# Performance work log

Measured on AMD Instinct MI355X. Metric: run time of the kernel, lower is better.

The kernel has to match this reference:

```python
import jax, jax.numpy as jnp
import numpy as np

# AdaMixer AdaptiveMixing config
G = 4          # n_groups
P_IN = 32      # in_points
P_OUT = 128    # out_points
C_EFF = 64     # eff_in_dim == eff_out_dim (in_dim=out_dim=256 / G)
DQ = 256       # query_dim
M_PARAMS = C_EFF * C_EFF      # 4096
S_PARAMS = P_IN * P_OUT       # 4096
TOTAL = M_PARAMS + S_PARAMS   # 8192
EPS = 1e-5


def setup_inputs() -> dict:
    key = jax.random.key(0)
    k = jax.random.split(key, 6)
    B, N = 8, 500
    x = jax.random.normal(k[0], (B, N, G, P_IN, C_EFF), dtype=jnp.float32)
    query = jax.random.normal(k[1], (B, N, DQ), dtype=jnp.float32)
    # parameter generator Linear(DQ -> G*TOTAL). (Original inits weight to zero;
    # we use small random weights so the computation is non-degenerate.)
    Wp = jax.random.normal(k[2], (G * TOTAL, DQ), dtype=jnp.float32) * 0.02
    bp = jax.random.normal(k[3], (G * TOTAL,), dtype=jnp.float32) * 0.02
    # out_proj Linear(G*P_OUT*C_EFF -> DQ)
    Wo = jax.random.normal(k[4], (DQ, G * P_OUT * C_EFF), dtype=jnp.float32) * 0.02
    bo = jax.random.normal(k[5], (DQ,), dtype=jnp.float32) * 0.02
    return {"x": x, "query": query, "Wp": Wp, "bp": bp, "Wo": Wo, "bo": bo}


def _ln2(t):
    # LayerNorm over last two axes, no affine (F.layer_norm(out, [P, C]))
    mean = jnp.mean(t, axis=(-2, -1), keepdims=True)
    var = jnp.var(t, axis=(-2, -1), keepdims=True)
    return (t - mean) * jax.lax.rsqrt(var + EPS)


def reference(x, query, Wp, bp, Wo, bo):
    B, N = query.shape[:2]
    # generate per-query mixing parameters: [B, N, G*TOTAL]
    params = jnp.einsum('bnd,pd->bnp', query, Wp) + bp
    params = params.reshape(B, N, G, TOTAL)
    M = params[..., :M_PARAMS].reshape(B, N, G, C_EFF, C_EFF)
    S = params[..., M_PARAMS:].reshape(B, N, G, P_OUT, P_IN)
    # adaptive channel mixing: [B,N,G,P_in,C] @ [B,N,G,C,C]
    out = jnp.einsum('bngpc,bngcd->bngpd', x, M)
    out = jax.nn.relu(_ln2(out))
    # adaptive spatial mixing: [B,N,G,P_out,P_in] @ [B,N,G,P_in,C]
    out = jnp.einsum('bngop,bngpc->bngoc', S, out)
    out = jax.nn.relu(_ln2(out))
    # output projection back to query dim + residual
    out = out.reshape(B, N, G * P_OUT * C_EFF)
    out = jnp.einsum('bnf,df->bnd', out, Wo) + bo
    return query + out
```

## Files before the change

kernel.cpp:

```cpp
#include <hip/hip_runtime.h>

typedef __attribute__((ext_vector_type(8))) __bf16 bf16x8;
typedef __attribute__((ext_vector_type(4))) float f32x4;
typedef __attribute__((ext_vector_type(8))) unsigned short u16x8;
typedef __attribute__((ext_vector_type(4))) unsigned short u16x4;
typedef unsigned int u32;

#define KS2 32

__device__ __forceinline__ unsigned short f2b(float f) {
    union { float f; unsigned u; } v; v.f = f;
    unsigned r = v.u + 0x7fffu + ((v.u >> 16) & 1u);
    return (unsigned short)(r >> 16);
}

__device__ __forceinline__ float b2f(unsigned short b) {
    union { unsigned u; float f; } v; v.u = ((unsigned)b) << 16;
    return v.f;
}

__device__ __forceinline__ bf16x8 ld_frag(const unsigned short* p) {
    u16x8 v = *(const u16x8*)p;
    return __builtin_bit_cast(bf16x8, v);
}

__device__ __forceinline__ void gl16(void* lds, const void* g) {
    __builtin_amdgcn_global_load_lds(
        (const __attribute__((address_space(1))) u32*)g,
        (__attribute__((address_space(3))) u32*)lds, 16, 0, 0);
}

#define WAIT_VM0 asm volatile("s_waitcnt vmcnt(0)" ::: "memory")
#define WAIT_VM3 asm volatile("s_waitcnt vmcnt(3)" ::: "memory")
#define WAIT_VM6 asm volatile("s_waitcnt vmcnt(6)" ::: "memory")
#define WAIT_LG0 asm volatile("s_waitcnt lgkmcnt(0)" ::: "memory")
#define BARRIER  __builtin_amdgcn_s_barrier()

__device__ __forceinline__ int inv_col(int j) {
    int off = j & 8191;
    return (off < 4096) ? ((j & ~8191) | ((off & 63) << 6) | (off >> 6)) : j;
}

__device__ __forceinline__ void block_reduce2(float& s, float& q, float* red) {
    for (int m = 1; m < 64; m <<= 1) { s += __shfl_xor(s, m); q += __shfl_xor(q, m); }
    int w = threadIdx.x >> 6;
    __syncthreads();
    if ((threadIdx.x & 63) == 0) { red[w] = s; red[w + 4] = q; }
    __syncthreads();
    s = red[0] + red[1] + red[2] + red[3];
    q = red[4] + red[5] + red[6] + red[7];
}

__global__ __launch_bounds__(256) void k_cvt(const float* __restrict__ src,
                                             unsigned short* __restrict__ dst, int n4) {
    int i = blockIdx.x * 256 + threadIdx.x;
    int stride = gridDim.x * 256;
    for (; i < n4; i += stride) {
        f32x4 v = *(const f32x4*)&src[(size_t)i * 4];
        u16x4 o = { f2b(v[0]), f2b(v[1]), f2b(v[2]), f2b(v[3]) };
        *(u16x4*)&dst[(size_t)i * 4] = o;
    }
}

__global__ __launch_bounds__(256) void k_cvt_wp(const float* __restrict__ Wp,
                                                unsigned short* __restrict__ Wpb, int n4) {
    int i = blockIdx.x * 256 + threadIdx.x;
    int stride = gridDim.x * 256;
    for (; i < n4; i += stride) {
        int e = i * 4;
        int j = e >> 8, k = e & 255;
        int jo = inv_col(j);
        f32x4 v = *(const f32x4*)&Wp[(size_t)jo * 256 + k];
        u16x4 o = { f2b(v[0]), f2b(v[1]), f2b(v[2]), f2b(v[3]) };
        *(u16x4*)&Wpb[(size_t)e] = o;
    }
}

__global__ __launch_bounds__(256) void k_perm_bp(const float* __restrict__ bp,
                                                 float* __restrict__ bpp) {
    int j = blockIdx.x * 256 + threadIdx.x;
    bpp[j] = bp[inv_col(j)];
}


__global__ __launch_bounds__(512) void k_gemm1(
    const unsigned short* __restrict__ qb, const unsigned short* __restrict__ Wpb,
    const float* __restrict__ bpp, unsigned short* __restrict__ pm, int CH)
{
    __shared__ char SB[73728];
    const int t = threadIdx.x, lane = t & 63, w = t >> 6;
    const int l15 = lane & 15, k8 = lane >> 4;
    const int n0 = blockIdx.x * 128, m0 = blockIdx.y * 256;
    const int wm = (w >> 1) * 64, wn = (w & 1) * 64;

    f32x4 acc[4][4];
    for (int i = 0; i < 4; ++i)
        for (int j = 0; j < 4; ++j) acc[i][j] = (f32x4){0.f, 0.f, 0.f, 0.f};

    const int r0 = t >> 2;
    const int cbs = (((t & 3) ^ (r0 & 3)) * 16);
    int ma0 = m0 + r0;        if (ma0 > CH - 1) ma0 = CH - 1;
    int ma1 = m0 + r0 + 128;  if (ma1 > CH - 1) ma1 = CH - 1;
    const char* pa0 = (const char*)qb  + (size_t)ma0 * 512 + cbs;
    const char* pa1 = (const char*)qb  + (size_t)ma1 * 512 + cbs;
    const char* pb0 = (const char*)Wpb + (size_t)(n0 + r0) * 512 + cbs;

    char* cur = SB;
    char* nx1 = SB + 24576;
    char* nx2 = SB + 49152;

    gl16(cur + t * 16,         pa0);
    gl16(cur + 8192 + t * 16,  pa1);
    gl16(cur + 16384 + t * 16, pb0);
    gl16(nx1 + t * 16,         pa0 + 64);
    gl16(nx1 + 8192 + t * 16,  pa1 + 64);
    gl16(nx1 + 16384 + t * 16, pb0 + 64);

    for (int kt = 0; kt < 8; ++kt) {
        if (kt < 6) {
            const int kb = (kt + 2) * 64;
            gl16(nx2 + t * 16,         pa0 + kb);
            gl16(nx2 + 8192 + t * 16,  pa1 + kb);
            gl16(nx2 + 16384 + t * 16, pb0 + kb);
            WAIT_VM6;
        } else if (kt == 6) {
            WAIT_VM3;
        } else {
            WAIT_VM0;
        }
        BARRIER;
        const unsigned short* Ab = (const unsigned short*)cur;
        const unsigned short* Bb = (const unsigned short*)(cur + 16384);
        bf16x8 a[4], b[4];
        for (int mi = 0; mi < 4; ++mi) {
            int row = wm + mi * 16 + l15;
            a[mi] = ld_frag(&Ab[row * 32 + (k8 ^ (row & 3)) * 8]);
        }
        for (int ni = 0; ni < 4; ++ni) {
            int row = wn + ni * 16 + l15;
            b[ni] = ld_frag(&Bb[row * 32 + (k8 ^ (row & 3)) * 8]);
        }
        WAIT_LG0;
        for (int mi = 0; mi < 4; ++mi)
            for (int ni = 0; ni < 4; ++ni)
                acc[mi][ni] = __builtin_amdgcn_mfma_f32_16x16x32_bf16(a[mi], b[ni], acc[mi][ni], 0, 0, 0);
        BARRIER;
        char* tmp = cur; cur = nx1; nx1 = nx2; nx2 = tmp;
    }

    unsigned short* Ep = (unsigned short*)SB;
    for (int ni = 0; ni < 4; ++ni) {
        int col = wn + ni * 16 + l15;
        float bpv = bpp[n0 + col];
        for (int mi = 0; mi < 4; ++mi)
            for (int r = 0; r < 4; ++r) {
                int row = wm + mi * 16 + k8 * 4 + r;
                Ep[row * 128 + col] = f2b(acc[mi][ni][r] + bpv);
            }
    }
    __syncthreads();
    for (int i = 0; i < 8; ++i) {
        int off = t * 16 + i * 8192;
        int row = off >> 8, colb = off & 255;
        int cm = m0 + row;
        if (cm < CH)
            *(u16x8*)((char*)pm + (size_t)cm * 65536 + (size_t)n0 * 2 + colb) =
                *(const u16x8*)((const char*)SB + off);
    }
}

__global__ __launch_bounds__(256) void k_mix(
    const float* __restrict__ x, unsigned short* __restrict__ pm, int q0)
{
    __shared__ char SB[29184];
    __shared__ float red[8];
    unsigned short* MtP = (unsigned short*)SB;
    unsigned short* Ax  = (unsigned short*)(SB + 9216);
    unsigned short* Ss  = (unsigned short*)(SB + 13824);
    unsigned short* O1  = (unsigned short*)(SB + 24064);
    unsigned short* O2  = (unsigned short*)SB;
    const int t = threadIdx.x, lane = t & 63, w = t >> 6;
    const int l15 = lane & 15, k8 = lane >> 4;
    const int g = blockIdx.x, nq = blockIdx.y;
    unsigned short* pmq = pm + (size_t)nq * 32768 + g * 8192;
    const float* xg = x + ((size_t)(q0 + nq) * 4 + g) * 2048;

    {
        int d = t >> 2, c0 = (t & 3) * 16;
        u16x8 v0 = *(const u16x8*)&pmq[d * 64 + c0];
        u16x8 v1 = *(const u16x8*)&pmq[d * 64 + c0 + 8];
        *(u16x8*)&MtP[d * 72 + c0] = v0;
        *(u16x8*)&MtP[d * 72 + c0 + 8] = v1;
    }
    {
        int o = t >> 1, p0 = (t & 1) * 16;
        u16x8 v0 = *(const u16x8*)&pmq[4096 + o * 32 + p0];
        u16x8 v1 = *(const u16x8*)&pmq[4096 + o * 32 + p0 + 8];
        *(u16x8*)&Ss[o * 40 + p0] = v0;
        *(u16x8*)&Ss[o * 40 + p0 + 8] = v1;
    }
    {
        int p = t >> 3, c0 = (t & 7) * 8;
        f32x4 v0 = *(const f32x4*)&xg[p * 64 + c0];
        f32x4 v1 = *(const f32x4*)&xg[p * 64 + c0 + 4];
        u16x8 o8 = { f2b(v0[0]), f2b(v0[1]), f2b(v0[2]), f2b(v0[3]),
                     f2b(v1[0]), f2b(v1[1]), f2b(v1[2]), f2b(v1[3]) };
        *(u16x8*)&Ax[p * 72 + c0] = o8;
    }
    __syncthreads();

    f32x4 acc1[2] = { (f32x4){0.f,0.f,0.f,0.f}, (f32x4){0.f,0.f,0.f,0.f} };
    for (int kk = 0; kk < 2; ++kk) {
        bf16x8 b = ld_frag(&MtP[(16 * w + l15) * 72 + kk * 32 + k8 * 8]);
        for (int mi = 0; mi < 2; ++mi) {
            bf16x8 a = ld_frag(&Ax[(mi * 16 + l15) * 72 + kk * 32 + k8 * 8]);
            acc1[mi] = __builtin_amdgcn_mfma_f32_16x16x32_bf16(a, b, acc1[mi], 0, 0, 0);
        }
    }
    float s = 0.f, sq = 0.f;
    for (int mi = 0; mi < 2; ++mi)
        for (int r = 0; r < 4; ++r) { float v = acc1[mi][r]; s += v; sq += v * v; }
    block_reduce2(s, sq, red);
    float mean = s * (1.f / 2048.f);
    float inv = rsqrtf(sq * (1.f / 2048.f) - mean * mean + 1e-5f);
    for (int mi = 0; mi < 2; ++mi)
        for (int r = 0; r < 4; ++r) {
            float v = (acc1[mi][r] - mean) * inv; v = fmaxf(v, 0.f);
            int p = mi * 16 + k8 * 4 + r, d = 16 * w + l15;
            O1[d * 40 + p] = f2b(v);
        }
    __syncthreads();

    f32x4 acc2[8];
    for (int mi = 0; mi < 8; ++mi) acc2[mi] = (f32x4){0.f, 0.f, 0.f, 0.f};
    bf16x8 b2 = ld_frag(&O1[(16 * w + l15) * 40 + k8 * 8]);
    for (int mi = 0; mi < 8; ++mi) {
        bf16x8 a2 = ld_frag(&Ss[(mi * 16 + l15) * 40 + k8 * 8]);
        acc2[mi] = __builtin_amdgcn_mfma_f32_16x16x32_bf16(a2, b2, acc2[mi], 0, 0, 0);
    }
    s = 0.f; sq = 0.f;
    for (int mi = 0; mi < 8; ++mi)
        for (int r = 0; r < 4; ++r) { float v = acc2[mi][r]; s += v; sq += v * v; }
    block_reduce2(s, sq, red);
    mean = s * (1.f / 8192.f);
    inv = rsqrtf(sq * (1.f / 8192.f) - mean * mean + 1e-5f);
    for (int mi = 0; mi < 8; ++mi)
        for (int r = 0; r < 4; ++r) {
            float v = (acc2[mi][r] - mean) * inv; v = fmaxf(v, 0.f);
            int o = mi * 16 + k8 * 4 + r, d = 16 * w + l15;
            O2[o * 64 + d] = f2b(v);
        }
    __syncthreads();
    for (int i = 0; i < 4; ++i) {
        int off = t * 16 + i * 4096;
        *(u16x8*)((char*)pmq + off) = *(const u16x8*)((const char*)O2 + off);
    }
}

__global__ __launch_bounds__(512) void k_gemm2(
    const unsigned short* __restrict__ pm, const unsigned short* __restrict__ Wob,
    unsigned short* __restrict__ part, int CH)
{
    __shared__ char SB[73728];
    const int t = threadIdx.x, lane = t & 63, w = t >> 6;
    const int l15 = lane & 15, k8 = lane >> 4;
    const int m0 = blockIdx.x * 128;
    const int ks = blockIdx.y;
    const int ksb = ks * (65536 / KS2);
    const int wm = (w >> 2) * 64, wn = (w & 3) * 64;

    f32x4 acc[4][4];
    for (int i = 0; i < 4; ++i)
        for (int j = 0; j < 4; ++j) acc[i][j] = (f32x4){0.f, 0.f, 0.f, 0.f};

    const int r0 = t >> 2;
    const int cbs = (((t & 3) ^ (r0 & 3)) * 16);
    int ma = m0 + r0; if (ma > CH - 1) ma = CH - 1;
    const char* pa  = (const char*)pm  + (size_t)ma * 65536 + ksb + cbs;
    const char* pb0 = (const char*)Wob + (size_t)r0 * 65536 + ksb + cbs;
    const char* pb1 = pb0 + (size_t)128 * 65536;

    char* cur = SB;
    char* nx1 = SB + 24576;
    char* nx2 = SB + 49152;

    gl16(cur + t * 16,          pa);
    gl16(cur + 8192 + t * 16,   pb0);
    gl16(cur + 16384 + t * 16,  pb1);
    gl16(nx1 + t * 16,          pa + 64);
    gl16(nx1 + 8192 + t * 16,   pb0 + 64);
    gl16(nx1 + 16384 + t * 16,  pb1 + 64);

    const int NT = (65536 / KS2) / 64;
    for (int kt = 0; kt < NT; ++kt) {
        if (kt < NT - 2) {
            const int kb = (kt + 2) * 64;
            gl16(nx2 + t * 16,         pa  + kb);
            gl16(nx2 + 8192 + t * 16,  pb0 + kb);
            gl16(nx2 + 16384 + t * 16, pb1 + kb);
            WAIT_VM6;
        } else if (kt == NT - 2) {
            WAIT_VM3;
        } else {
            WAIT_VM0;
        }
        BARRIER;
        const unsigned short* Ab = (const unsigned short*)cur;
        const unsigned short* Bb = (const unsigned short*)(cur + 8192);
        bf16x8 a[4], b[4];
        for (int mi = 0; mi < 4; ++mi) {
            int row = wm + mi * 16 + l15;
            a[mi] = ld_frag(&Ab[row * 32 + (k8 ^ (row & 3)) * 8]);
        }
        for (int ni = 0; ni < 4; ++ni) {
            int row = wn + ni * 16 + l15;
            b[ni] = ld_frag(&Bb[row * 32 + (k8 ^ (row & 3)) * 8]);
        }
        WAIT_LG0;
        for (int mi = 0; mi < 4; ++mi)
            for (int ni = 0; ni < 4; ++ni)
                acc[mi][ni] = __builtin_amdgcn_mfma_f32_16x16x32_bf16(a[mi], b[ni], acc[mi][ni], 0, 0, 0);
        BARRIER;
        char* tmp = cur; cur = nx1; nx1 = nx2; nx2 = tmp;
    }

    for (int mi = 0; mi < 4; ++mi)
        for (int ni = 0; ni < 4; ++ni)
            for (int r = 0; r < 4; ++r) {
                int row = wm + mi * 16 + k8 * 4 + r;
                int cm = m0 + row;
                int d = wn + ni * 16 + l15;
                if (cm < CH) part[((size_t)ks * CH + cm) * 256 + d] = f2b(acc[mi][ni][r]);
            }
}

__global__ __launch_bounds__(256) void k_reduce(
    const unsigned short* __restrict__ part, const float* __restrict__ query,
    const float* __restrict__ bo, float* __restrict__ out, int q0, int CH)
{
    int row = blockIdx.x * 4 + (threadIdx.x >> 6);
    if (row >= CH) return;
    int d4 = (threadIdx.x & 63) * 4;
    f32x4 s = *(const f32x4*)&bo[d4];
    f32x4 qv = *(const f32x4*)&query[(size_t)(q0 + row) * 256 + d4];
    s = s + qv;
    for (int ks = 0; ks < KS2; ++ks) {
        u16x4 p4 = *(const u16x4*)&part[((size_t)ks * CH + row) * 256 + d4];
        s[0] += b2f(p4[0]); s[1] += b2f(p4[1]); s[2] += b2f(p4[2]); s[3] += b2f(p4[3]);
    }
    *(f32x4*)&out[(size_t)(q0 + row) * 256 + d4] = s;
}

extern "C" void kernel_launch(void* const* d_in, const int* in_sizes, int n_in,
                              void* d_out, int out_size, void* d_ws, size_t ws_size,
                              hipStream_t stream) {
    const float* x     = (const float*)d_in[0];
    const float* query = (const float*)d_in[1];
    const float* Wp    = (const float*)d_in[2];
    const float* bp    = (const float*)d_in[3];
    const float* Wo    = (const float*)d_in[4];
    const float* bo    = (const float*)d_in[5];
    float* out = (float*)d_out;

    char* ws = (char*)d_ws;
    unsigned short* Wpb = (unsigned short*)ws;
    unsigned short* Wob = (unsigned short*)(ws + 16777216);
    unsigned short* qb  = (unsigned short*)(ws + 33554432);
    float*          bpp = (float*)(ws + 35602432);
    char* chunkbase = ws + 35733504;
    const size_t fixed = 35733504;

    static const int cands[] = {2000, 1000, 500, 250, 200, 125, 100, 50, 25, 20, 10, 8, 5, 4, 2, 1};
    int CH = 1;
    for (int i = 0; i < (int)(sizeof(cands) / sizeof(cands[0])); ++i) {
        size_t need = fixed + (size_t)cands[i] * (65536 + (size_t)KS2 * 512);
        if (need <= ws_size) { CH = cands[i]; break; }
    }
    unsigned short* pm = (unsigned short*)chunkbase;
    unsigned short* part = (unsigned short*)(chunkbase + (size_t)CH * 65536);
    const int NC = 4000 / CH;

    k_perm_bp<<<128, 256, 0, stream>>>(bp, bpp);
    k_cvt_wp<<<2048, 256, 0, stream>>>(Wp, Wpb, 32768 * 256 / 4);
    k_cvt<<<2048, 256, 0, stream>>>(Wo, Wob, 256 * 32768 / 4);
    k_cvt<<<1000, 256, 0, stream>>>(query, qb, 4000 * 256 / 4);

    for (int c = 0; c < NC; ++c) {
        int q0 = c * CH;
        k_gemm1<<<dim3(256, (CH + 255) / 256), 512, 0, stream>>>(
            qb + (size_t)q0 * 256, Wpb, bpp, pm, CH);
        k_mix<<<dim3(4, CH), 256, 0, stream>>>(x, pm, q0);
        k_gemm2<<<dim3((CH + 127) / 128, KS2), 512, 0, stream>>>(pm, Wob, part, CH);
        k_reduce<<<dim3((CH + 3) / 4), 256, 0, stream>>>(part, query, bo, out, q0, CH);
    }
}
```

Measured before the change: 349.8 us.

## Enlarge gemm2 M tile to 256 and map K-splits to XCDs

The output-projection split-K GEMM now uses a 256-row M tile per block (8x4 MFMA accumulators per wave) instead of 128, so each Wo tile loaded into LDS serves twice as many rows. The grid is flattened to 1D and remapped so that consecutive block IDs, which land on different XCDs, take different K-splits while blocks sharing a K-split share an XCD and its L2. This cuts Wo global traffic and block count, at the cost of more accumulator registers, more LDS (96KB), and fewer blocks, which can lower occupancy.

After: 353.2 us. About the same (+1.0%).

```diff
diff --git a/kernel.cpp b/kernel.cpp
--- a/kernel.cpp
+++ b/kernel.cpp
@@ -32,7 +32,9 @@
 
 #define WAIT_VM0 asm volatile("s_waitcnt vmcnt(0)" ::: "memory")
 #define WAIT_VM3 asm volatile("s_waitcnt vmcnt(3)" ::: "memory")
+#define WAIT_VM4 asm volatile("s_waitcnt vmcnt(4)" ::: "memory")
 #define WAIT_VM6 asm volatile("s_waitcnt vmcnt(6)" ::: "memory")
+#define WAIT_VM8 asm volatile("s_waitcnt vmcnt(8)" ::: "memory")
 #define WAIT_LG0 asm volatile("s_waitcnt lgkmcnt(0)" ::: "memory")
 #define BARRIER  __builtin_amdgcn_s_barrier()
 
@@ -259,56 +261,63 @@
 
 __global__ __launch_bounds__(512) void k_gemm2(
     const unsigned short* __restrict__ pm, const unsigned short* __restrict__ Wob,
-    unsigned short* __restrict__ part, int CH)
+    unsigned short* __restrict__ part, int CH, int MB2)
 {
-    __shared__ char SB[73728];
+    __shared__ char SB[98304];
     const int t = threadIdx.x, lane = t & 63, w = t >> 6;
     const int l15 = lane & 15, k8 = lane >> 4;
-    const int m0 = blockIdx.x * 128;
-    const int ks = blockIdx.y;
+    const int bid = blockIdx.x;
+    const int xcd = bid & 7, local = bid >> 3;
+    const int ks = xcd + 8 * (local / MB2);
+    const int m0 = (local % MB2) * 256;
     const int ksb = ks * (65536 / KS2);
-    const int wm = (w >> 2) * 64, wn = (w & 3) * 64;
-
-    f32x4 acc[4][4];
-    for (int i = 0; i < 4; ++i)
+    const int wm = (w >> 2) * 128, wn = (w & 3) * 64;
+
+    f32x4 acc[8][4];
+    for (int i = 0; i < 8; ++i)
         for (int j = 0; j < 4; ++j) acc[i][j] = (f32x4){0.f, 0.f, 0.f, 0.f};
 
     const int r0 = t >> 2;
     const int cbs = (((t & 3) ^ (r0 & 3)) * 16);
-    int ma = m0 + r0; if (ma > CH - 1) ma = CH - 1;
-    const char* pa  = (const char*)pm  + (size_t)ma * 65536 + ksb + cbs;
+    int ma0 = m0 + r0;        if (ma0 > CH - 1) ma0 = CH - 1;
+    int ma1 = m0 + r0 + 128;  if (ma1 > CH - 1) ma1 = CH - 1;
+    const char* pa0 = (const char*)pm  + (size_t)ma0 * 65536 + ksb + cbs;
+    const char* pa1 = (const char*)pm  + (size_t)ma1 * 65536 + ksb + cbs;
     const char* pb0 = (const char*)Wob + (size_t)r0 * 65536 + ksb + cbs;
     const char* pb1 = pb0 + (size_t)128 * 65536;
 
     char* cur = SB;
-    char* nx1 = SB + 24576;
-    char* nx2 = SB + 49152;
-
-    gl16(cur + t * 16,          pa);
-    gl16(cur + 8192 + t * 16,   pb0);
-    gl16(cur + 16384 + t * 16,  pb1);
-    gl16(nx1 + t * 16,          pa + 64);
-    gl16(nx1 + 8192 + t * 16,   pb0 + 64);
-    gl16(nx1 + 16384 + t * 16,  pb1 + 64);
+    char* nx1 = SB + 32768;
+    char* nx2 = SB + 65536;
+
+    gl16(cur + t * 16,          pa0);
+    gl16(cur + 8192 + t * 16,   pa1);
+    gl16(cur + 16384 + t * 16,  pb0);
+    gl16(cur + 24576 + t * 16,  pb1);
+    gl16(nx1 + t * 16,          pa0 + 64);
+    gl16(nx1 + 8192 + t * 16,   pa1 + 64);
+    gl16(nx1 + 16384 + t * 16,  pb0 + 64);
+    gl16(nx1 + 24576 + t * 16,  pb1 + 64);
 
     const int NT = (65536 / KS2) / 64;
     for (int kt = 0; kt < NT; ++kt) {
         if (kt < NT - 2) {
             const int kb = (kt + 2) * 64;
-            gl16(nx2 + t * 16,         pa  + kb);
-            gl16(nx2 + 8192 + t * 16,  pb0 + kb);
-            gl16(nx2 + 16384 + t * 16, pb1 + kb);
-            WAIT_VM6;
+            gl16(nx2 + t * 16,          pa0 + kb);
+            gl16(nx2 + 8192 + t * 16,   pa1 + kb);
+            gl16(nx2 + 16384 + t * 16,  pb0 + kb);
+            gl16(nx2 + 24576 + t * 16,  pb1 + kb);
+            WAIT_VM8;
         } else if (kt == NT - 2) {
-            WAIT_VM3;
+            WAIT_VM4;
         } else {
             WAIT_VM0;
         }
         BARRIER;
         const unsigned short* Ab = (const unsigned short*)cur;
-        const unsigned short* Bb = (const unsigned short*)(cur + 8192);
-        bf16x8 a[4], b[4];
-        for (int mi = 0; mi < 4; ++mi) {
+        const unsigned short* Bb = (const unsigned short*)(cur + 16384);
+        bf16x8 a[8], b[4];
+        for (int mi = 0; mi < 8; ++mi) {
             int row = wm + mi * 16 + l15;
             a[mi] = ld_frag(&Ab[row * 32 + (k8 ^ (row & 3)) * 8]);
         }
@@ -317,14 +326,14 @@
             b[ni] = ld_frag(&Bb[row * 32 + (k8 ^ (row & 3)) * 8]);
         }
         WAIT_LG0;
-        for (int mi = 0; mi < 4; ++mi)
+        for (int mi = 0; mi < 8; ++mi)
             for (int ni = 0; ni < 4; ++ni)
                 acc[mi][ni] = __builtin_amdgcn_mfma_f32_16x16x32_bf16(a[mi], b[ni], acc[mi][ni], 0, 0, 0);
         BARRIER;
         char* tmp = cur; cur = nx1; nx1 = nx2; nx2 = tmp;
     }
 
-    for (int mi = 0; mi < 4; ++mi)
+    for (int mi = 0; mi < 8; ++mi)
         for (int ni = 0; ni < 4; ++ni)
             for (int r = 0; r < 4; ++r) {
                 int row = wm + mi * 16 + k8 * 4 + r;
@@ -387,10 +396,11 @@
 
     for (int c = 0; c < NC; ++c) {
         int q0 = c * CH;
+        const int MB2 = (CH + 255) / 256;
         k_gemm1<<<dim3(256, (CH + 255) / 256), 512, 0, stream>>>(
             qb + (size_t)q0 * 256, Wpb, bpp, pm, CH);
         k_mix<<<dim3(4, CH), 256, 0, stream>>>(x, pm, q0);
-        k_gemm2<<<dim3((CH + 127) / 128, KS2), 512, 0, stream>>>(pm, Wob, part, CH);
+        k_gemm2<<<dim3(KS2 * MB2), 512, 0, stream>>>(pm, Wob, part, CH, MB2);
         k_reduce<<<dim3((CH + 3) / 4), 256, 0, stream>>>(part, query, bo, out, q0, CH);
     }
 }
```

## Store intermediate and Wo in K-split blocked layout for contiguous split-K loads

Applied to the files above, without the earlier changes.

Re-lays the per-query intermediate buffer and the bf16 copy of Wo so that each of the 32 K-slices (1024 elements) is stored as a contiguous [rows x 2048-byte] block. gemm1, mix and gemm2 index into this blocked layout, and a new conversion kernel permutes Wo into it. The aim is to give the split-K gemm2 rows that sit close together in memory, instead of 64 KB row strides, which should improve DRAM page and TLB locality. The cost is more scattered writes in gemm1 and mix, plus extra index arithmetic.

Result: no change. 349.1 us (-0.2%).

```diff
diff --git a/kernel.cpp b/kernel.cpp
--- a/kernel.cpp
+++ b/kernel.cpp
@@ -76,6 +76,22 @@
     }
 }
 
+__global__ __launch_bounds__(256) void k_cvt_wo(const float* __restrict__ Wo,
+                                                unsigned short* __restrict__ Wob, int n4) {
+    int i = blockIdx.x * 256 + threadIdx.x;
+    int stride = gridDim.x * 256;
+    for (; i < n4; i += stride) {
+        int e = i * 4;
+        int off = e & 1023;
+        int rowidx = e >> 10;
+        int d = rowidx & 255;
+        int ks = rowidx >> 8;
+        f32x4 v = *(const f32x4*)&Wo[(size_t)d * 32768 + ks * 1024 + off];
+        u16x4 o = { f2b(v[0]), f2b(v[1]), f2b(v[2]), f2b(v[3]) };
+        *(u16x4*)&Wob[(size_t)e] = o;
+    }
+}
+
 __global__ __launch_bounds__(256) void k_perm_bp(const float* __restrict__ bp,
                                                  float* __restrict__ bpp) {
     int j = blockIdx.x * 256 + threadIdx.x;
@@ -159,18 +175,20 @@
             }
     }
     __syncthreads();
+    const int ksg = n0 >> 10;
+    const int cb0 = (n0 & 1023) * 2;
     for (int i = 0; i < 8; ++i) {
         int off = t * 16 + i * 8192;
         int row = off >> 8, colb = off & 255;
         int cm = m0 + row;
         if (cm < CH)
-            *(u16x8*)((char*)pm + (size_t)cm * 65536 + (size_t)n0 * 2 + colb) =
+            *(u16x8*)((char*)pm + ((size_t)ksg * CH + cm) * 2048 + cb0 + colb) =
                 *(const u16x8*)((const char*)SB + off);
     }
 }
 
 __global__ __launch_bounds__(256) void k_mix(
-    const float* __restrict__ x, unsigned short* __restrict__ pm, int q0)
+    const float* __restrict__ x, unsigned short* __restrict__ pm, int q0, int CH)
 {
     __shared__ char SB[29184];
     __shared__ float red[8];
@@ -182,20 +200,25 @@
     const int t = threadIdx.x, lane = t & 63, w = t >> 6;
     const int l15 = lane & 15, k8 = lane >> 4;
     const int g = blockIdx.x, nq = blockIdx.y;
-    unsigned short* pmq = pm + (size_t)nq * 32768 + g * 8192;
+    char* pmb = (char*)pm;
+    const size_t rowb = 2048;
     const float* xg = x + ((size_t)(q0 + nq) * 4 + g) * 2048;
 
     {
         int d = t >> 2, c0 = (t & 3) * 16;
-        u16x8 v0 = *(const u16x8*)&pmq[d * 64 + c0];
-        u16x8 v1 = *(const u16x8*)&pmq[d * 64 + c0 + 8];
+        const char* src = pmb + ((size_t)(g * 8 + (d >> 4)) * CH + nq) * rowb
+                              + ((d & 15) * 64 + c0) * 2;
+        u16x8 v0 = *(const u16x8*)(src);
+        u16x8 v1 = *(const u16x8*)(src + 16);
         *(u16x8*)&MtP[d * 72 + c0] = v0;
         *(u16x8*)&MtP[d * 72 + c0 + 8] = v1;
     }
     {
         int o = t >> 1, p0 = (t & 1) * 16;
-        u16x8 v0 = *(const u16x8*)&pmq[4096 + o * 32 + p0];
-        u16x8 v1 = *(const u16x8*)&pmq[4096 + o * 32 + p0 + 8];
+        const char* src = pmb + ((size_t)(g * 8 + 4 + (o >> 5)) * CH + nq) * rowb
+                              + ((o & 31) * 32 + p0) * 2;
+        u16x8 v0 = *(const u16x8*)(src);
+        u16x8 v1 = *(const u16x8*)(src + 16);
         *(u16x8*)&Ss[o * 40 + p0] = v0;
         *(u16x8*)&Ss[o * 40 + p0 + 8] = v1;
     }
@@ -253,7 +276,10 @@
     __syncthreads();
     for (int i = 0; i < 4; ++i) {
         int off = t * 16 + i * 4096;
-        *(u16x8*)((char*)pmq + off) = *(const u16x8*)((const char*)O2 + off);
+        int elem = off >> 1;
+        char* dst = pmb + ((size_t)(g * 8 + (elem >> 10)) * CH + nq) * rowb
+                        + (elem & 1023) * 2;
+        *(u16x8*)dst = *(const u16x8*)((const char*)O2 + off);
     }
 }
 
@@ -266,7 +292,6 @@
     const int l15 = lane & 15, k8 = lane >> 4;
     const int m0 = blockIdx.x * 128;
     const int ks = blockIdx.y;
-    const int ksb = ks * (65536 / KS2);
     const int wm = (w >> 2) * 64, wn = (w & 3) * 64;
 
     f32x4 acc[4][4];
@@ -276,9 +301,9 @@
     const int r0 = t >> 2;
     const int cbs = (((t & 3) ^ (r0 & 3)) * 16);
     int ma = m0 + r0; if (ma > CH - 1) ma = CH - 1;
-    const char* pa  = (const char*)pm  + (size_t)ma * 65536 + ksb + cbs;
-    const char* pb0 = (const char*)Wob + (size_t)r0 * 65536 + ksb + cbs;
-    const char* pb1 = pb0 + (size_t)128 * 65536;
+    const char* pa  = (const char*)pm  + ((size_t)ks * CH + ma) * 2048 + cbs;
+    const char* pb0 = (const char*)Wob + ((size_t)ks * 256 + r0) * 2048 + cbs;
+    const char* pb1 = pb0 + (size_t)128 * 2048;
 
     char* cur = SB;
     char* nx1 = SB + 24576;
@@ -291,7 +316,7 @@
     gl16(nx1 + 8192 + t * 16,   pb0 + 64);
     gl16(nx1 + 16384 + t * 16,  pb1 + 64);
 
-    const int NT = (65536 / KS2) / 64;
+    const int NT = 2048 / 64;
     for (int kt = 0; kt < NT; ++kt) {
         if (kt < NT - 2) {
             const int kb = (kt + 2) * 64;
@@ -382,14 +407,14 @@
 
     k_perm_bp<<<128, 256, 0, stream>>>(bp, bpp);
     k_cvt_wp<<<2048, 256, 0, stream>>>(Wp, Wpb, 32768 * 256 / 4);
-    k_cvt<<<2048, 256, 0, stream>>>(Wo, Wob, 256 * 32768 / 4);
+    k_cvt_wo<<<2048, 256, 0, stream>>>(Wo, Wob, 256 * 32768 / 4);
     k_cvt<<<1000, 256, 0, stream>>>(query, qb, 4000 * 256 / 4);
 
     for (int c = 0; c < NC; ++c) {
         int q0 = c * CH;
         k_gemm1<<<dim3(256, (CH + 255) / 256), 512, 0, stream>>>(
             qb + (size_t)q0 * 256, Wpb, bpp, pm, CH);
-        k_mix<<<dim3(4, CH), 256, 0, stream>>>(x, pm, q0);
+        k_mix<<<dim3(4, CH), 256, 0, stream>>>(x, pm, q0, CH);
         k_gemm2<<<dim3((CH + 127) / 128, KS2), 512, 0, stream>>>(pm, Wob, part, CH);
         k_reduce<<<dim3((CH + 3) / 4), 256, 0, stream>>>(part, query, bo, out, q0, CH);
     }
```
